# Performance work log

Measured on AMD Instinct MI355X. Metric: run time of the kernel, lower is better.

Reference implementation:

```python
import jax, jax.numpy as jnp
import numpy as np

EMBED_DIM = 1024
NUM_HEADS = 16
HEAD_DIM = EMBED_DIM // NUM_HEADS
SCALE = HEAD_DIM ** -0.5


def setup_inputs() -> dict:
    key = jax.random.key(0)
    k_x, k_wqkv, k_wp, k_bp = jax.random.split(key, 4)
    B, N, C = 4, 2048, EMBED_DIM
    x = jax.random.normal(k_x, (B, N, C), dtype=jnp.float32)
    # nn.Linear(C, 3C, bias=False): weight shape (3C, C), y = x @ W.T
    w_qkv = jax.random.normal(k_wqkv, (3 * C, C), dtype=jnp.float32) * (C ** -0.5)
    # nn.Linear(C, C) with bias
    w_proj = jax.random.normal(k_wp, (C, C), dtype=jnp.float32) * (C ** -0.5)
    b_proj = jax.random.normal(k_bp, (C,), dtype=jnp.float32) * 0.02
    return {"x": x, "w_qkv": w_qkv, "w_proj": w_proj, "b_proj": b_proj}


def reference(x, w_qkv, w_proj, b_proj):
    B, N, C = x.shape
    H, D = NUM_HEADS, HEAD_DIM
    # qkv: (B, N, 3C) -> (3, B, H, N, D)
    qkv = jnp.einsum('bnc,ec->bne', x, w_qkv)
    qkv = qkv.reshape(B, N, 3, H, D).transpose(2, 0, 3, 1, 4)
    q, k, v = qkv[0], qkv[1], qkv[2]
    attn = jnp.einsum('bhnd,bhmd->bhnm', q, k) * SCALE
    attn = jax.nn.softmax(attn, axis=-1)  # dropout p=0.0 -> identity
    out = jnp.einsum('bhnm,bhmd->bhnd', attn, v)
    out = out.transpose(0, 2, 1, 3).reshape(B, N, C)
    out = jnp.einsum('bnc,oc->bno', out, w_proj) + b_proj
    return out
```

## Files before the change

### kernel.cpp

```cpp
#include <hip/hip_runtime.h>

typedef unsigned short u16;
typedef u16 u16x8 __attribute__((ext_vector_type(8)));
typedef u16 u16x4 __attribute__((ext_vector_type(4)));
typedef unsigned u32x4 __attribute__((ext_vector_type(4)));
typedef float f32x4 __attribute__((ext_vector_type(4)));
typedef float f32x16 __attribute__((ext_vector_type(16)));
typedef __bf16 bf16x8 __attribute__((ext_vector_type(8)));

#define QSCALE_LOG2E 0.18033688011112042f

__device__ __forceinline__ u16 cvt_bf16(float f) {
  __bf16 h = (__bf16)f;
  return __builtin_bit_cast(u16, h);
}

__device__ __forceinline__ void gl_lds16(const void* g, void* l) {
  __builtin_amdgcn_global_load_lds(
      (const __attribute__((address_space(1))) void*)g,
      (__attribute__((address_space(3))) void*)l, 16, 0, 0);
}

__global__ __launch_bounds__(256) void cast_f32_bf16(const float* __restrict__ in,
                                                     u16* __restrict__ out) {
  long i = ((long)blockIdx.x * 256 + threadIdx.x) * 8;
  f32x4 a = *(const f32x4*)(in + i);
  f32x4 b = *(const f32x4*)(in + i + 4);
  u16x8 o;
  o[0] = cvt_bf16(a[0]); o[1] = cvt_bf16(a[1]); o[2] = cvt_bf16(a[2]); o[3] = cvt_bf16(a[3]);
  o[4] = cvt_bf16(b[0]); o[5] = cvt_bf16(b[1]); o[6] = cvt_bf16(b[2]); o[7] = cvt_bf16(b[3]);
  *(u16x8*)(out + i) = o;
}

template<int MODE>
__global__ __launch_bounds__(256) void gemm_nt(
    const u16* __restrict__ A, const u16* __restrict__ Bw,
    u16* __restrict__ Cb, u16* __restrict__ Vt,
    float* __restrict__ Cf, const float* __restrict__ bias) {
  constexpr int K = 1024;
  __shared__ __align__(16) u16 sA[128 * 32];
  __shared__ __align__(16) u16 sB[128 * 32];
  const int t = threadIdx.x;
  const int w = t >> 6, l = t & 63;
  const int fr = l & 15, fg = l >> 4;
  const int bm = blockIdx.y * 128, bn = blockIdx.x * 128;
  const int wr = (w >> 1) << 6, wc = (w & 1) << 6;

  f32x4 acc[4][4] = {};

  const int tr = t >> 2, tc = (t & 3) * 8;
  const u16* gA0 = A + (long)(bm + tr) * K + tc;
  const u16* gB0 = Bw + (long)(bn + tr) * K + tc;
  char* sAc = (char*)sA; char* sBc = (char*)sB;
  const int wb = w * 1024;

  for (int k0 = 0; k0 < K; k0 += 32) {
    gl_lds16(gA0 + k0,                 sAc + wb);
    gl_lds16(gA0 + (long)64 * K + k0,  sAc + 4096 + wb);
    gl_lds16(gB0 + k0,                 sBc + wb);
    gl_lds16(gB0 + (long)64 * K + k0,  sBc + 4096 + wb);
    __syncthreads();
    bf16x8 af[4], bf[4];
#pragma unroll
    for (int m = 0; m < 4; ++m)
      af[m] = *(const bf16x8*)&sA[(wr + m * 16 + fr) * 32 + fg * 8];
#pragma unroll
    for (int n = 0; n < 4; ++n)
      bf[n] = *(const bf16x8*)&sB[(wc + n * 16 + fr) * 32 + fg * 8];
#pragma unroll
    for (int m = 0; m < 4; ++m) {
#pragma unroll
      for (int n = 0; n < 4; ++n)
        acc[m][n] = __builtin_amdgcn_mfma_f32_16x16x32_bf16(af[m], bf[n], acc[m][n], 0, 0, 0);
    }
    __syncthreads();
  }

  const float cmul = (MODE == 0 && bn < 1024) ? QSCALE_LOG2E : 1.0f;
#pragma unroll
  for (int m = 0; m < 4; ++m) {
    const int grow = bm + wr + m * 16 + fg * 4;
#pragma unroll
    for (int n = 0; n < 4; ++n) {
      const int gcol = bn + wc + n * 16 + fr;
      if (MODE == 1) {
        float bv = bias[gcol];
#pragma unroll
        for (int r = 0; r < 4; ++r)
          Cf[(long)(grow + r) * 1024 + gcol] = acc[m][n][r] + bv;
      } else {
        if (bn < 2048) {
#pragma unroll
          for (int r = 0; r < 4; ++r)
            Cb[(long)(grow + r) * 2048 + gcol] = cvt_bf16(acc[m][n][r] * cmul);
        } else {
          const int d = gcol - 2048;
          const int bb = grow >> 11, nn = grow & 2047;
          u16x4 pk;
#pragma unroll
          for (int r = 0; r < 4; ++r) pk[r] = cvt_bf16(acc[m][n][r]);
          *(u16x4*)&Vt[((long)(bb * 16 + (d >> 6)) * 64 + (d & 63)) * 2048 + nn] = pk;
        }
      }
    }
  }
}

__global__ __launch_bounds__(512, 4) void attn_fused(
    const u16* __restrict__ qk, const u16* __restrict__ vt,
    u16* __restrict__ ao) {
  const int t = threadIdx.x;
  const int w = t >> 6, l = t & 63;
  const int hi = l >> 5, ql = l & 31;
  const int bi = blockIdx.x;
  const int bh = (bi & 7) * 8 + ((bi >> 3) & 7);
  const int qt = bi >> 6;
  const int b = bh >> 4, h = bh & 15;
  const int qbase = qt * 256 + w * 32;

  __shared__ __align__(16) u16 sK[2][4096];
  __shared__ __align__(16) u16 sV[2][4096];
  __shared__ float sRed[8][32];

  bf16x8 qf[4];
  {
    const u16* qb = qk + (long)(b * 2048 + qbase + ql) * 2048 + h * 64 + hi * 8;
#pragma unroll
    for (int c = 0; c < 4; ++c) qf[c] = *(const bf16x8*)(qb + c * 16);
  }

  const int srow = w * 8 + (l >> 3);
  const int schunk = (l & 7) ^ (l >> 3);
  const u16* gKs = qk + (long)(b * 2048 + srow) * 2048 + 1024 + h * 64 + schunk * 8;
  const u16* gVs = vt + (long)(bh * 64 + srow) * 2048 + schunk * 8;
  char* sKc = (char*)sK; char* sVc = (char*)sV;
  const int wb = w * 1024;

  auto STAGE = [&](int buf, int kv0) {
    gl_lds16(gKs + (long)kv0 * 2048, sKc + buf * 8192 + wb);
    gl_lds16(gVs + kv0,              sVc + buf * 8192 + wb);
  };

  f32x16 acc0 = {}, acc1 = {};
  float mrow = -__builtin_inff(), lrow = 0.f;

  STAGE(0, 0);
  __syncthreads();
  int cur = 0;

  for (int ti = 0; ti < 32; ++ti) {
    if (ti < 31) STAGE(cur ^ 1, (ti + 1) * 64);

    f32x16 s0 = {}, s1 = {};
#pragma unroll
    for (int c = 0; c < 4; ++c) {
      bf16x8 kf = *(const bf16x8*)&sK[cur][(0 * 32 + ql) * 64 + (((2 * c + hi) ^ (l & 7)) * 8)];
      s0 = __builtin_amdgcn_mfma_f32_32x32x16_bf16(kf, qf[c], s0, 0, 0, 0);
    }
#pragma unroll
    for (int c = 0; c < 4; ++c) {
      bf16x8 kf = *(const bf16x8*)&sK[cur][(1 * 32 + ql) * 64 + (((2 * c + hi) ^ (l & 7)) * 8)];
      s1 = __builtin_amdgcn_mfma_f32_32x32x16_bf16(kf, qf[c], s1, 0, 0, 0);
    }

    float mloc = s0[0];
#pragma unroll
    for (int r = 1; r < 16; ++r) mloc = fmaxf(mloc, s0[r]);
#pragma unroll
    for (int r = 0; r < 16; ++r) mloc = fmaxf(mloc, s1[r]);
    mloc = fmaxf(mloc, __shfl_xor(mloc, 32));
    float nm = fmaxf(mrow, mloc);
    if (!__all(nm - mrow <= 8.0f)) {
      float al = __builtin_amdgcn_exp2f(mrow - nm);
      lrow *= al;
      mrow = nm;
      if (l < 32) sRed[w][ql] = al;
#pragma unroll
      for (int r = 0; r < 16; ++r) {
        float a2 = sRed[w][(r & 3) + 8 * (r >> 2) + 4 * hi];
        acc0[r] *= a2;
        acc1[r] *= a2;
      }
    }
    float ls = 0.f;
#pragma unroll
    for (int r = 0; r < 16; ++r) { float p = __builtin_amdgcn_exp2f(s0[r] - mrow); s0[r] = p; ls += p; }
#pragma unroll
    for (int r = 0; r < 16; ++r) { float p = __builtin_amdgcn_exp2f(s1[r] - mrow); s1[r] = p; ls += p; }
    ls += __shfl_xor(ls, 32);
    lrow += ls;

    bf16x8 pa[2][2];
    {
      unsigned W[8];
#pragma unroll
      for (int ii = 0; ii < 8; ++ii)
        asm("v_cvt_pk_bf16_f32 %0, %1, %2" : "=v"(W[ii]) : "v"(s0[2 * ii]), "v"(s0[2 * ii + 1]));
      asm("v_permlane32_swap_b32 %0, %1" : "+v"(W[0]), "+v"(W[2]));
      asm("v_permlane32_swap_b32 %0, %1" : "+v"(W[1]), "+v"(W[3]));
      asm("v_permlane32_swap_b32 %0, %1" : "+v"(W[4]), "+v"(W[6]));
      asm("v_permlane32_swap_b32 %0, %1" : "+v"(W[5]), "+v"(W[7]));
      u32x4 f0 = {W[0], W[1], W[2], W[3]}, f1 = {W[4], W[5], W[6], W[7]};
      pa[0][0] = __builtin_bit_cast(bf16x8, f0);
      pa[0][1] = __builtin_bit_cast(bf16x8, f1);
    }
    {
      unsigned W[8];
#pragma unroll
      for (int ii = 0; ii < 8; ++ii)
        asm("v_cvt_pk_bf16_f32 %0, %1, %2" : "=v"(W[ii]) : "v"(s1[2 * ii]), "v"(s1[2 * ii + 1]));
      asm("v_permlane32_swap_b32 %0, %1" : "+v"(W[0]), "+v"(W[2]));
      asm("v_permlane32_swap_b32 %0, %1" : "+v"(W[1]), "+v"(W[3]));
      asm("v_permlane32_swap_b32 %0, %1" : "+v"(W[4]), "+v"(W[6]));
      asm("v_permlane32_swap_b32 %0, %1" : "+v"(W[5]), "+v"(W[7]));
      u32x4 f0 = {W[0], W[1], W[2], W[3]}, f1 = {W[4], W[5], W[6], W[7]};
      pa[1][0] = __builtin_bit_cast(bf16x8, f0);
      pa[1][1] = __builtin_bit_cast(bf16x8, f1);
    }

#pragma unroll
    for (int kt = 0; kt < 2; ++kt) {
#pragma unroll
      for (int kc = 0; kc < 2; ++kc) {
        bf16x8 v0 = *(const bf16x8*)&sV[cur][(0 * 32 + ql) * 64 + (((4 * kt + 2 * kc + hi) ^ (l & 7)) * 8)];
        acc0 = __builtin_amdgcn_mfma_f32_32x32x16_bf16(pa[kt][kc], v0, acc0, 0, 0, 0);
        bf16x8 v1 = *(const bf16x8*)&sV[cur][(1 * 32 + ql) * 64 + (((4 * kt + 2 * kc + hi) ^ (l & 7)) * 8)];
        acc1 = __builtin_amdgcn_mfma_f32_32x32x16_bf16(pa[kt][kc], v1, acc1, 0, 0, 0);
      }
    }
    __syncthreads();
    cur ^= 1;
  }

  if (l < 32) sRed[w][ql] = 1.0f / lrow;
  __builtin_amdgcn_s_waitcnt(0);
#pragma unroll
  for (int r = 0; r < 16; ++r) {
    const int qr = (r & 3) + 8 * (r >> 2) + 4 * hi;
    const float inv = sRed[w][qr];
    u16* ob = ao + (long)(b * 2048 + qbase + qr) * 1024 + h * 64 + ql;
    ob[0]  = cvt_bf16(acc0[r] * inv);
    ob[32] = cvt_bf16(acc1[r] * inv);
  }
}

extern "C" void kernel_launch(void* const* d_in, const int* in_sizes, int n_in,
                              void* d_out, int out_size, void* d_ws, size_t ws_size,
                              hipStream_t stream) {
  const float* x     = (const float*)d_in[0];
  const float* wqkv  = (const float*)d_in[1];
  const float* wproj = (const float*)d_in[2];
  const float* bproj = (const float*)d_in[3];
  float* out = (float*)d_out;

  u16* ws    = (u16*)d_ws;
  u16* xb    = ws;
  u16* wqkvb = xb + 8388608;
  u16* wpb   = wqkvb + 3145728;
  u16* qkb   = wpb + 1048576;
  u16* vtb   = qkb + 16777216;
  u16* aob   = xb;

  cast_f32_bf16<<<4096, 256, 0, stream>>>(x, xb);
  cast_f32_bf16<<<1536, 256, 0, stream>>>(wqkv, wqkvb);
  cast_f32_bf16<<<512, 256, 0, stream>>>(wproj, wpb);

  gemm_nt<0><<<dim3(24, 64), 256, 0, stream>>>(xb, wqkvb, qkb, vtb, nullptr, nullptr);
  attn_fused<<<512, 512, 0, stream>>>(qkb, vtb, aob);
  gemm_nt<1><<<dim3(8, 64), 256, 0, stream>>>(aob, wpb, nullptr, nullptr, out, bproj);
}
```

Measured before the change: 278.6 us.

## Replace QKV GEMM with 256x256-tile, 8-wave, double-buffered pipelined kernel

The QKV projection now uses a dedicated kernel with 256x256 tiles, 512 threads and K-step 64. LDS is double-buffered and XOR-swizzled, and the staging of the next tile is split into parts interleaved with MFMA phases. Explicit vmcnt waits, barriers and s_setprio raise MFMA priority, and a grid remap groups blocks by XCD. This targets the low arithmetic intensity and exposed load latency of the old 128x128 single-buffer loop, at the cost of higher register and LDS pressure and a hand-scheduled barrier sequence.

```diff
diff --git a/kernel.cpp b/kernel.cpp
--- a/kernel.cpp
+++ b/kernel.cpp
@@ -20,6 +20,13 @@
       (const __attribute__((address_space(1))) void*)g,
       (__attribute__((address_space(3))) void*)l, 16, 0, 0);
 }
+
+#define SBAR() __builtin_amdgcn_s_barrier()
+#define SCHED0() __builtin_amdgcn_sched_barrier(0)
+#define VMCNT2() asm volatile("s_waitcnt vmcnt(2)" ::: "memory")
+#define VMCNT0() asm volatile("s_waitcnt vmcnt(0)" ::: "memory")
+#define PRIO1() __builtin_amdgcn_s_setprio(1)
+#define PRIO0() __builtin_amdgcn_s_setprio(0)
 
 __global__ __launch_bounds__(256) void cast_f32_bf16(const float* __restrict__ in,
                                                      u16* __restrict__ out) {
@@ -32,10 +39,155 @@
   *(u16x8*)(out + i) = o;
 }
 
-template<int MODE>
-__global__ __launch_bounds__(256) void gemm_nt(
+__global__ __launch_bounds__(512, 2) void gemm1_8p(
     const u16* __restrict__ A, const u16* __restrict__ Bw,
-    u16* __restrict__ Cb, u16* __restrict__ Vt,
+    u16* __restrict__ Cb, u16* __restrict__ Vt) {
+  constexpr int K = 1024;
+  __shared__ __align__(16) u16 sA[2][2][8192];
+  __shared__ __align__(16) u16 sB[2][2][8192];
+
+  const int t = threadIdx.x;
+  const int w = t >> 6, l = t & 63;
+  const int fr = l & 15, fg = l >> 4;
+  const int wm = w >> 2, wn = w & 3;
+
+  const int bid = blockIdx.x;
+  const int xcd = bid & 7, c = bid >> 3;
+  const int by = xcd * 4 + (c & 3), bx = c >> 2;
+  const int bm = by * 256, bn = bx * 256;
+
+  const int strow = t >> 3;
+  const int scol8 = (t & 7) ^ (strow & 7);
+  const u16* gAs = A + (long)(bm + strow) * K + scol8 * 8;
+  const u16* gBs = Bw + (long)(bn + strow) * K + scol8 * 8;
+
+#define STAGE_PART(d, part, kt)                                          \
+  do {                                                                   \
+    const int mh_ = (part) & 1;                                          \
+    const long off_ = (long)(mh_ * 128) * K + (long)(kt) * 64;           \
+    if ((part) < 2) {                                                    \
+      char* dst_ = (char*)&sA[d][mh_][0] + w * 1024;                     \
+      gl_lds16(gAs + off_,          dst_);                               \
+      gl_lds16(gAs + off_ + 64 * K, dst_ + 8192);                        \
+    } else {                                                             \
+      char* dst_ = (char*)&sB[d][mh_][0] + w * 1024;                     \
+      gl_lds16(gBs + off_,          dst_);                               \
+      gl_lds16(gBs + off_ + 64 * K, dst_ + 8192);                        \
+    }                                                                    \
+  } while (0)
+
+#define LDA4(af, d, mq, kk)                                              \
+  do {                                                                   \
+    const u16* b_ = &sA[d][wm][0];                                       \
+    _Pragma("unroll")                                                    \
+    for (int mi_ = 0; mi_ < 4; ++mi_) {                                  \
+      const int row_ = ((mq)*4 + mi_) * 16 + fr;                         \
+      af[mi_] = *(const bf16x8*)&b_[row_ * 64 + ((((kk)*4 + fg) ^ (fr & 7)) * 8)]; \
+    }                                                                    \
+  } while (0)
+
+#define LDB4(bf, d, kk)                                                  \
+  do {                                                                   \
+    const u16* b_ = &sB[d][wn >> 1][0];                                  \
+    _Pragma("unroll")                                                    \
+    for (int ni_ = 0; ni_ < 4; ++ni_) {                                  \
+      const int row_ = (wn & 1) * 64 + ni_ * 16 + fr;                    \
+      bf[ni_] = *(const bf16x8*)&b_[row_ * 64 + ((((kk)*4 + fg) ^ (fr & 7)) * 8)]; \
+    }                                                                    \
+  } while (0)
+
+#define MFMA16(af, bf, mq)                                               \
+  do {                                                                   \
+    PRIO1();                                                             \
+    _Pragma("unroll")                                                    \
+    for (int mi_ = 0; mi_ < 4; ++mi_) {                                  \
+      _Pragma("unroll")                                                  \
+      for (int ni_ = 0; ni_ < 4; ++ni_)                                  \
+        acc[(mq)*4 + mi_][ni_] = __builtin_amdgcn_mfma_f32_16x16x32_bf16( \
+            af[mi_], bf[ni_], acc[(mq)*4 + mi_][ni_], 0, 0, 0);          \
+    }                                                                    \
+    PRIO0();                                                             \
+  } while (0)
+
+  f32x4 acc[8][4] = {};
+  bf16x8 a4[4], b4[4];
+
+  STAGE_PART(0, 0, 0); STAGE_PART(0, 1, 0); STAGE_PART(0, 2, 0); STAGE_PART(0, 3, 0);
+
+  for (int it = 0; it < 8; ++it) {
+    const int ktb = 2 * it + 1;
+    const int ktn = 2 * it + 2;
+    STAGE_PART(1, 0, ktb);
+    VMCNT2(); SBAR(); SCHED0();
+    LDB4(b4, 0, 0); LDA4(a4, 0, 0, 0);
+    MFMA16(a4, b4, 0);
+    SBAR();
+    LDA4(a4, 0, 1, 0);
+    STAGE_PART(1, 1, ktb);
+    SBAR();
+    MFMA16(a4, b4, 1);
+    SBAR();
+    LDB4(b4, 0, 1); LDA4(a4, 0, 0, 1);
+    STAGE_PART(1, 2, ktb);
+    SBAR();
+    MFMA16(a4, b4, 0);
+    SBAR();
+    LDA4(a4, 0, 1, 1);
+    STAGE_PART(1, 3, ktb);
+    SBAR();
+    MFMA16(a4, b4, 1);
+    SBAR();
+    if (it < 7) { STAGE_PART(0, 0, ktn); VMCNT2(); } else { VMCNT0(); }
+    SBAR(); SCHED0();
+    LDB4(b4, 1, 0); LDA4(a4, 1, 0, 0);
+    MFMA16(a4, b4, 0);
+    SBAR();
+    LDA4(a4, 1, 1, 0);
+    if (it < 7) STAGE_PART(0, 1, ktn);
+    SBAR();
+    MFMA16(a4, b4, 1);
+    SBAR();
+    LDB4(b4, 1, 1); LDA4(a4, 1, 0, 1);
+    if (it < 7) STAGE_PART(0, 2, ktn);
+    SBAR();
+    MFMA16(a4, b4, 0);
+    SBAR();
+    LDA4(a4, 1, 1, 1);
+    if (it < 7) STAGE_PART(0, 3, ktn);
+    SBAR();
+    MFMA16(a4, b4, 1);
+    SBAR();
+  }
+
+  const float cmul = (bn < 1024) ? QSCALE_LOG2E : 1.0f;
+#pragma unroll
+  for (int mi = 0; mi < 8; ++mi) {
+    const int grow = bm + wm * 128 + mi * 16 + fg * 4;
+#pragma unroll
+    for (int ni = 0; ni < 4; ++ni) {
+      const int gcol = bn + wn * 64 + ni * 16 + fr;
+      if (bn < 2048) {
+#pragma unroll
+        for (int r = 0; r < 4; ++r)
+          Cb[(long)(grow + r) * 2048 + gcol] = cvt_bf16(acc[mi][ni][r] * cmul);
+      } else {
+        const int d = gcol - 2048;
+        const int bb = grow >> 11, nn = grow & 2047;
+        u16x4 pk;
+#pragma unroll
+        for (int r = 0; r < 4; ++r) pk[r] = cvt_bf16(acc[mi][ni][r]);
+        *(u16x4*)&Vt[((long)(bb * 16 + (d >> 6)) * 64 + (d & 63)) * 2048 + nn] = pk;
+      }
+    }
+  }
+#undef STAGE_PART
+#undef LDA4
+#undef LDB4
+#undef MFMA16
+}
+
+__global__ __launch_bounds__(256) void gemm_nt_proj(
+    const u16* __restrict__ A, const u16* __restrict__ Bw,
     float* __restrict__ Cf, const float* __restrict__ bias) {
   constexpr int K = 1024;
   __shared__ __align__(16) u16 sA[128 * 32];
@@ -76,32 +228,16 @@
     __syncthreads();
   }
 
-  const float cmul = (MODE == 0 && bn < 1024) ? QSCALE_LOG2E : 1.0f;
 #pragma unroll
   for (int m = 0; m < 4; ++m) {
     const int grow = bm + wr + m * 16 + fg * 4;
 #pragma unroll
     for (int n = 0; n < 4; ++n) {
       const int gcol = bn + wc + n * 16 + fr;
-      if (MODE == 1) {
-        float bv = bias[gcol];
-#pragma unroll
-        for (int r = 0; r < 4; ++r)
-          Cf[(long)(grow + r) * 1024 + gcol] = acc[m][n][r] + bv;
-      } else {
-        if (bn < 2048) {
-#pragma unroll
-          for (int r = 0; r < 4; ++r)
-            Cb[(long)(grow + r) * 2048 + gcol] = cvt_bf16(acc[m][n][r] * cmul);
-        } else {
-          const int d = gcol - 2048;
-          const int bb = grow >> 11, nn = grow & 2047;
-          u16x4 pk;
-#pragma unroll
-          for (int r = 0; r < 4; ++r) pk[r] = cvt_bf16(acc[m][n][r]);
-          *(u16x4*)&Vt[((long)(bb * 16 + (d >> 6)) * 64 + (d & 63)) * 2048 + nn] = pk;
-        }
-      }
+      float bv = bias[gcol];
+#pragma unroll
+      for (int r = 0; r < 4; ++r)
+        Cf[(long)(grow + r) * 1024 + gcol] = acc[m][n][r] + bv;
     }
   }
 }
@@ -129,6 +265,9 @@
     for (int c = 0; c < 4; ++c) qf[c] = *(const bf16x8*)(qb + c * 16);
   }
 
+  f32x16 acc0 = {}, acc1 = {};
+  float mrow = -__builtin_inff(), lrow = 0.f;
+
   const int srow = w * 8 + (l >> 3);
   const int schunk = (l & 7) ^ (l >> 3);
   const u16* gKs = qk + (long)(b * 2048 + srow) * 2048 + 1024 + h * 64 + schunk * 8;
@@ -140,9 +279,6 @@
     gl_lds16(gKs + (long)kv0 * 2048, sKc + buf * 8192 + wb);
     gl_lds16(gVs + kv0,              sVc + buf * 8192 + wb);
   };
-
-  f32x16 acc0 = {}, acc1 = {};
-  float mrow = -__builtin_inff(), lrow = 0.f;
 
   STAGE(0, 0);
   __syncthreads();
@@ -265,7 +401,7 @@
   cast_f32_bf16<<<1536, 256, 0, stream>>>(wqkv, wqkvb);
   cast_f32_bf16<<<512, 256, 0, stream>>>(wproj, wpb);
 
-  gemm_nt<0><<<dim3(24, 64), 256, 0, stream>>>(xb, wqkvb, qkb, vtb, nullptr, nullptr);
+  gemm1_8p<<<384, 512, 0, stream>>>(xb, wqkvb, qkb, vtb);
   attn_fused<<<512, 512, 0, stream>>>(qkb, vtb, aob);
-  gemm_nt<1><<<dim3(8, 64), 256, 0, stream>>>(aob, wpb, nullptr, nullptr, out, bproj);
-}
+  gemm_nt_proj<<<dim3(8, 64), 256, 0, stream>>>(aob, wpb, out, bproj);
+}
```

Result: no change. 280.4 us (+0.6%).

## Replace QKV projection GEMM with 256x256-tile 8-wave pingpong-pipelined kernel

Applied to the files above, without the earlier changes.

The QKV projection GEMM moves from a 128x128 tile, 256-thread, single-buffered kernel to a 256x256 tile, 512-thread kernel. It double-buffers LDS, uses a swizzled layout, and interleaves async global-to-LDS loads with MFMA quarters under explicit vmcnt waits, barriers and setprio. The aim is to hide global load latency behind MFMA work and raise operand reuse per tile, cutting memory stalls in the largest GEMM. It also remaps block IDs so blocks are grouped across XCDs. In exchange the hand-scheduled barriers bring higher register and LDS pressure and more fragile ordering, and the grid shrinks to 384 blocks.

```diff
diff --git a/kernel.cpp b/kernel.cpp
--- a/kernel.cpp
+++ b/kernel.cpp
@@ -20,6 +20,13 @@
       (const __attribute__((address_space(1))) void*)g,
       (__attribute__((address_space(3))) void*)l, 16, 0, 0);
 }
+
+#define SBAR() __builtin_amdgcn_s_barrier()
+#define SCHED0() __builtin_amdgcn_sched_barrier(0)
+#define VMCNT6() asm volatile("s_waitcnt vmcnt(6)" ::: "memory")
+#define VMCNT0() asm volatile("s_waitcnt vmcnt(0)" ::: "memory")
+#define PRIO1() __builtin_amdgcn_s_setprio(1)
+#define PRIO0() __builtin_amdgcn_s_setprio(0)
 
 __global__ __launch_bounds__(256) void cast_f32_bf16(const float* __restrict__ in,
                                                      u16* __restrict__ out) {
@@ -32,10 +39,148 @@
   *(u16x8*)(out + i) = o;
 }
 
-template<int MODE>
-__global__ __launch_bounds__(256) void gemm_nt(
+__global__ __launch_bounds__(512, 2) void gemm1_8p(
     const u16* __restrict__ A, const u16* __restrict__ Bw,
-    u16* __restrict__ Cb, u16* __restrict__ Vt,
+    u16* __restrict__ Cb, u16* __restrict__ Vt) {
+  constexpr int K = 1024;
+  __shared__ __align__(16) u16 sA[2][2][8192];
+  __shared__ __align__(16) u16 sB[2][2][8192];
+
+  const int t = threadIdx.x;
+  const int w = t >> 6, l = t & 63;
+  const int fr = l & 15, fg = l >> 4;
+  const int wm = w >> 2, wn = w & 3;
+
+  const int bid = blockIdx.x;
+  const int xcd = bid & 7, c = bid >> 3;
+  const int by = xcd * 4 + (c & 3), bx = c >> 2;
+  const int bm = by * 256, bn = bx * 256;
+
+  const int strow = t >> 3;
+  const int scol8 = (t & 7) ^ (strow & 7);
+  const u16* gAs = A + (long)(bm + strow) * K + scol8 * 8;
+  const u16* gBs = Bw + (long)(bn + strow) * K + scol8 * 8;
+
+#define STAGE_A(bf_, mh_, kt_)                                           \
+  do {                                                                   \
+    char* d_ = (char*)&sA[bf_][mh_][0] + w * 1024;                       \
+    const u16* s_ = gAs + (long)((mh_) * 128) * K + (long)(kt_) * 64;    \
+    gl_lds16(s_,          d_);                                           \
+    gl_lds16(s_ + 64 * K, d_ + 8192);                                    \
+  } while (0)
+
+#define STAGE_B(bf_, nh_, kt_)                                           \
+  do {                                                                   \
+    char* d_ = (char*)&sB[bf_][nh_][0] + w * 1024;                       \
+    const u16* s_ = gBs + (long)((nh_) * 128) * K + (long)(kt_) * 64;    \
+    gl_lds16(s_,          d_);                                           \
+    gl_lds16(s_ + 64 * K, d_ + 8192);                                    \
+  } while (0)
+
+#define READ_A(bf_, mh_)                                                 \
+  do {                                                                   \
+    const u16* p_ = &sA[bf_][mh_][0];                                    \
+    _Pragma("unroll")                                                    \
+    for (int mi_ = 0; mi_ < 4; ++mi_) {                                  \
+      const int row_ = wm * 64 + mi_ * 16 + fr;                          \
+      _Pragma("unroll")                                                  \
+      for (int kk_ = 0; kk_ < 2; ++kk_)                                  \
+        af[mi_][kk_] = *(const bf16x8*)&p_[row_ * 64 + (((kk_ * 4 + fg) ^ (fr & 7)) * 8)]; \
+    }                                                                    \
+  } while (0)
+
+#define READ_B(bf_, nh_)                                                 \
+  do {                                                                   \
+    const u16* p_ = &sB[bf_][nh_][0];                                    \
+    _Pragma("unroll")                                                    \
+    for (int ni_ = 0; ni_ < 2; ++ni_) {                                  \
+      const int row_ = wn * 32 + ni_ * 16 + fr;                          \
+      _Pragma("unroll")                                                  \
+      for (int kk_ = 0; kk_ < 2; ++kk_)                                  \
+        bfr[nh_][ni_][kk_] = *(const bf16x8*)&p_[row_ * 64 + (((kk_ * 4 + fg) ^ (fr & 7)) * 8)]; \
+    }                                                                    \
+  } while (0)
+
+#define MFMAQ(mh_, nh_)                                                  \
+  do {                                                                   \
+    PRIO1();                                                             \
+    _Pragma("unroll")                                                    \
+    for (int mi_ = 0; mi_ < 4; ++mi_) {                                  \
+      _Pragma("unroll")                                                  \
+      for (int ni_ = 0; ni_ < 2; ++ni_) {                                \
+        _Pragma("unroll")                                                \
+        for (int kk_ = 0; kk_ < 2; ++kk_)                                \
+          acc[(mh_) * 4 + mi_][(nh_) * 2 + ni_] =                        \
+              __builtin_amdgcn_mfma_f32_16x16x32_bf16(                   \
+                  af[mi_][kk_], bfr[nh_][ni_][kk_],                      \
+                  acc[(mh_) * 4 + mi_][(nh_) * 2 + ni_], 0, 0, 0);       \
+      }                                                                  \
+    }                                                                    \
+    PRIO0();                                                             \
+  } while (0)
+
+  f32x4 acc[8][4] = {};
+  bf16x8 af[4][2], bfr[2][2][2];
+
+  STAGE_A(0, 0, 0); STAGE_B(0, 0, 0); STAGE_A(0, 1, 0); STAGE_B(0, 1, 0);
+  STAGE_A(1, 0, 1); STAGE_B(1, 0, 1);
+
+  for (int i = 0; i < 7; ++i) {
+    const int ktb = 2 * i + 1, ktn = 2 * i + 2, ktn1 = 2 * i + 3;
+    STAGE_A(1, 1, ktb); VMCNT6(); SBAR(); SCHED0();
+    READ_A(0, 0); READ_B(0, 0); MFMAQ(0, 0); SBAR();
+    READ_B(0, 1); STAGE_B(1, 1, ktb); SBAR(); MFMAQ(0, 1); SBAR();
+    READ_A(0, 1); STAGE_A(0, 0, ktn); SBAR(); MFMAQ(1, 0); SBAR();
+    STAGE_B(0, 0, ktn); SBAR(); MFMAQ(1, 1); SBAR();
+    STAGE_A(0, 1, ktn); VMCNT6(); SBAR(); SCHED0();
+    READ_A(1, 0); READ_B(1, 0); MFMAQ(0, 0); SBAR();
+    READ_B(1, 1); STAGE_B(0, 1, ktn); SBAR(); MFMAQ(0, 1); SBAR();
+    READ_A(1, 1); STAGE_A(1, 0, ktn1); SBAR(); MFMAQ(1, 0); SBAR();
+    STAGE_B(1, 0, ktn1); SBAR(); MFMAQ(1, 1); SBAR();
+  }
+  STAGE_A(1, 1, 15); VMCNT6(); SBAR(); SCHED0();
+  READ_A(0, 0); READ_B(0, 0); MFMAQ(0, 0); SBAR();
+  READ_B(0, 1); STAGE_B(1, 1, 15); SBAR(); MFMAQ(0, 1); SBAR();
+  READ_A(0, 1); SBAR(); MFMAQ(1, 0); SBAR();
+  SBAR(); MFMAQ(1, 1); SBAR();
+  VMCNT0(); SBAR(); SCHED0();
+  READ_A(1, 0); READ_B(1, 0); MFMAQ(0, 0); SBAR();
+  READ_B(1, 1); SBAR(); MFMAQ(0, 1); SBAR();
+  READ_A(1, 1); SBAR(); MFMAQ(1, 0); SBAR();
+  SBAR(); MFMAQ(1, 1); SBAR();
+
+  const float cmul = (bn < 1024) ? QSCALE_LOG2E : 1.0f;
+#pragma unroll
+  for (int mi = 0; mi < 8; ++mi) {
+    const int mh = mi >> 2, mi_ = mi & 3;
+    const int grow = bm + mh * 128 + wm * 64 + mi_ * 16 + fg * 4;
+#pragma unroll
+    for (int ni = 0; ni < 4; ++ni) {
+      const int nh = ni >> 1, ni_ = ni & 1;
+      const int gcol = bn + nh * 128 + wn * 32 + ni_ * 16 + fr;
+      if (bn < 2048) {
+#pragma unroll
+        for (int r = 0; r < 4; ++r)
+          Cb[(long)(grow + r) * 2048 + gcol] = cvt_bf16(acc[mi][ni][r] * cmul);
+      } else {
+        const int d = gcol - 2048;
+        const int bb = grow >> 11, nn = grow & 2047;
+        u16x4 pk;
+#pragma unroll
+        for (int r = 0; r < 4; ++r) pk[r] = cvt_bf16(acc[mi][ni][r]);
+        *(u16x4*)&Vt[((long)(bb * 16 + (d >> 6)) * 64 + (d & 63)) * 2048 + nn] = pk;
+      }
+    }
+  }
+#undef STAGE_A
+#undef STAGE_B
+#undef READ_A
+#undef READ_B
+#undef MFMAQ
+}
+
+__global__ __launch_bounds__(256) void gemm_nt_proj(
+    const u16* __restrict__ A, const u16* __restrict__ Bw,
     float* __restrict__ Cf, const float* __restrict__ bias) {
   constexpr int K = 1024;
   __shared__ __align__(16) u16 sA[128 * 32];
@@ -76,32 +221,16 @@
     __syncthreads();
   }
 
-  const float cmul = (MODE == 0 && bn < 1024) ? QSCALE_LOG2E : 1.0f;
 #pragma unroll
   for (int m = 0; m < 4; ++m) {
     const int grow = bm + wr + m * 16 + fg * 4;
 #pragma unroll
     for (int n = 0; n < 4; ++n) {
       const int gcol = bn + wc + n * 16 + fr;
-      if (MODE == 1) {
-        float bv = bias[gcol];
-#pragma unroll
-        for (int r = 0; r < 4; ++r)
-          Cf[(long)(grow + r) * 1024 + gcol] = acc[m][n][r] + bv;
-      } else {
-        if (bn < 2048) {
-#pragma unroll
-          for (int r = 0; r < 4; ++r)
-            Cb[(long)(grow + r) * 2048 + gcol] = cvt_bf16(acc[m][n][r] * cmul);
-        } else {
-          const int d = gcol - 2048;
-          const int bb = grow >> 11, nn = grow & 2047;
-          u16x4 pk;
-#pragma unroll
-          for (int r = 0; r < 4; ++r) pk[r] = cvt_bf16(acc[m][n][r]);
-          *(u16x4*)&Vt[((long)(bb * 16 + (d >> 6)) * 64 + (d & 63)) * 2048 + nn] = pk;
-        }
-      }
+      float bv = bias[gcol];
+#pragma unroll
+      for (int r = 0; r < 4; ++r)
+        Cf[(long)(grow + r) * 1024 + gcol] = acc[m][n][r] + bv;
     }
   }
 }
@@ -129,6 +258,9 @@
     for (int c = 0; c < 4; ++c) qf[c] = *(const bf16x8*)(qb + c * 16);
   }
 
+  f32x16 acc0 = {}, acc1 = {};
+  float mrow = -__builtin_inff(), lrow = 0.f;
+
   const int srow = w * 8 + (l >> 3);
   const int schunk = (l & 7) ^ (l >> 3);
   const u16* gKs = qk + (long)(b * 2048 + srow) * 2048 + 1024 + h * 64 + schunk * 8;
@@ -140,9 +272,6 @@
     gl_lds16(gKs + (long)kv0 * 2048, sKc + buf * 8192 + wb);
     gl_lds16(gVs + kv0,              sVc + buf * 8192 + wb);
   };
-
-  f32x16 acc0 = {}, acc1 = {};
-  float mrow = -__builtin_inff(), lrow = 0.f;
 
   STAGE(0, 0);
   __syncthreads();
@@ -265,7 +394,7 @@
   cast_f32_bf16<<<1536, 256, 0, stream>>>(wqkv, wqkvb);
   cast_f32_bf16<<<512, 256, 0, stream>>>(wproj, wpb);
 
-  gemm_nt<0><<<dim3(24, 64), 256, 0, stream>>>(xb, wqkvb, qkb, vtb, nullptr, nullptr);
+  gemm1_8p<<<384, 512, 0, stream>>>(xb, wqkvb, qkb, vtb);
   attn_fused<<<512, 512, 0, stream>>>(qkb, vtb, aob);
-  gemm_nt<1><<<dim3(8, 64), 256, 0, stream>>>(aob, wpb, nullptr, nullptr, out, bproj);
-}
+  gemm_nt_proj<<<dim3(8, 64), 256, 0, stream>>>(aob, wpb, out, bproj);
+}
```

Result: no change. 277.8 us (-0.3%).
